# Performance work log

Hardware: AMD Instinct MI355X
Metric: run time of the kernel (lower is better)

## Reference

```python
import jax, jax.numpy as jnp
import numpy as np


def layer_norm(x, w, b, eps=1e-5):
    mu = jnp.mean(x, axis=-1, keepdims=True)
    var = jnp.mean(jnp.square(x - mu), axis=-1, keepdims=True)
    return (x - mu) / jnp.sqrt(var + eps) * w + b


def setup_inputs() -> dict:
    B, T, S, D, K = 8, 2048, 2048, 512, 3
    ks = jax.random.split(jax.random.key(0), 8)
    w_scale = 0.02  # modest init so softmax/layernorm stay in a sane range
    return {
        "x": jax.random.normal(ks[0], (B, T, D), jnp.float32),
        "enc": jax.random.normal(ks[1], (B, S, D), jnp.float32),
        "conv_w": jax.random.normal(ks[2], (2 * D, D, K), jnp.float32) * w_scale,
        "conv_b": jnp.zeros((2 * D,), jnp.float32),
        "ln1_w": jnp.ones((D,), jnp.float32),
        "ln1_b": jnp.zeros((D,), jnp.float32),
        "Wq": jax.random.normal(ks[3], (D, D), jnp.float32) * w_scale,
        "bq": jnp.zeros((D,), jnp.float32),
        "Wk": jax.random.normal(ks[4], (D, D), jnp.float32) * w_scale,
        "bk": jnp.zeros((D,), jnp.float32),
        "Wv": jax.random.normal(ks[5], (D, D), jnp.float32) * w_scale,
        "bv": jnp.zeros((D,), jnp.float32),
        "Wo": jax.random.normal(ks[6], (D, D), jnp.float32) * w_scale,
        "bo": jnp.zeros((D,), jnp.float32),
        "ln2_w": jnp.ones((D,), jnp.float32),
        "ln2_b": jnp.zeros((D,), jnp.float32),
    }


def reference(x, enc, conv_w, conv_b, ln1_w, ln1_b, Wq, bq, Wk, bk, Wv, bv, Wo, bo, ln2_w, ln2_b):
    D = x.shape[-1]
    K = conv_w.shape[-1]
    # Causal GLU: left-pad by K-1 so each output sees only past/current positions.
    xt = jnp.transpose(x, (0, 2, 1))  # [B, D, T]
    xt = jnp.pad(xt, ((0, 0), (0, 0), (K - 1, 0)))
    conv = jax.lax.conv_general_dilated(
        xt, conv_w, window_strides=(1,), padding="VALID",
        dimension_numbers=("NCH", "OIH", "NCH"))
    conv = conv + conv_b[None, :, None]
    conv = jnp.transpose(conv, (0, 2, 1))  # [B, T, 2D]
    a, g = jnp.split(conv, 2, axis=-1)
    glu = a * jax.nn.sigmoid(g)
    # residual + LN1 (dropout is identity in eval mode)
    h = layer_norm(glu + x, ln1_w, ln1_b)
    # cross-attention: bmm -> softmax -> bmm (single head)
    q = h @ Wq.T + bq            # [B, T, D]
    k = enc @ Wk.T + bk          # [B, S, D]
    v = enc @ Wv.T + bv          # [B, S, D]
    scores = jnp.einsum("btd,bsd->bts", q, k) / jnp.sqrt(jnp.float32(D))
    attn = jax.nn.softmax(scores, axis=-1)  # [B, T, S]
    ctx = jnp.einsum("bts,bsd->btd", attn, v)
    ctx = ctx @ Wo.T + bo
    out = layer_norm(h + ctx, ln2_w, ln2_b)
    return out, attn
```

## Files before the change

kernel.cpp:

```cpp
#include <hip/hip_runtime.h>
#include <hip/hip_bf16.h>
#include <stdint.h>


typedef unsigned short ushortT;
typedef __bf16 bf16x8 __attribute__((ext_vector_type(8)));
typedef float floatx4 __attribute__((ext_vector_type(4)));
typedef unsigned short ushort4v __attribute__((ext_vector_type(4)));
typedef unsigned short ushort8 __attribute__((ext_vector_type(8)));

__device__ __forceinline__ ushortT f2bf(float f) {
  unsigned u = __builtin_bit_cast(unsigned, f);
  u += 0x7FFFu + ((u >> 16) & 1u);
  return (ushortT)(u >> 16);
}
__device__ __forceinline__ float bf2f(ushortT u) {
  return __builtin_bit_cast(float, (unsigned)u << 16);
}

__device__ __forceinline__ void gload_lds16(const void* g, void* l) {
  __builtin_amdgcn_global_load_lds(
      (const __attribute__((address_space(1))) void*)g,
      (__attribute__((address_space(3))) void*)l, 16, 0, 0);
}

__global__ __launch_bounds__(256)
void k_f32_to_bf16v(const float* __restrict__ src, ushortT* __restrict__ dst, long n4) {
  long i = (long)blockIdx.x * 256 + threadIdx.x;
  if (i >= n4) return;
  floatx4 v = *(const floatx4*)&src[i * 4];
  ushort4v o;
#pragma unroll
  for (int j = 0; j < 4; j++) o[j] = f2bf(v[j]);
  *(ushort4v*)&dst[i * 4] = o;
}

__global__ __launch_bounds__(256)
void k_w4(const float* __restrict__ w0, const float* __restrict__ w1,
          const float* __restrict__ w2, const float* __restrict__ w3,
          ushortT* __restrict__ dst) {
  long i = (long)blockIdx.x * 256 + threadIdx.x;
  int m = (int)(i >> 16);
  long within = (i & 65535) * 4;
  const float* s = (m == 0) ? w0 : (m == 1) ? w1 : (m == 2) ? w2 : w3;
  floatx4 v = *(const floatx4*)&s[within];
  ushort4v o;
#pragma unroll
  for (int j = 0; j < 4; j++) o[j] = f2bf(v[j]);
  *(ushort4v*)&dst[(long)m * 262144 + within] = o;
}

__global__ __launch_bounds__(128)
void k_xpad(const float* __restrict__ x, ushortT* __restrict__ xp) {
  int row = blockIdx.x;
  int b = row / 2050, tp = row % 2050;
  int c = threadIdx.x * 4;
  ushort4v o = {0, 0, 0, 0};
  if (tp >= 2) {
    floatx4 v = *(const floatx4*)&x[((long)(b * 2048 + tp - 2)) * 512 + c];
#pragma unroll
    for (int j = 0; j < 4; j++) o[j] = f2bf(v[j]);
  }
  *(ushort4v*)&xp[(long)row * 512 + c] = o;
}

__global__ __launch_bounds__(256)
void k_convw(const float* __restrict__ w, ushortT* __restrict__ dst) {
  long idx = (long)blockIdx.x * 256 + threadIdx.x;
  if (idx >= 1024L * 1536) return;
  int n = (int)(idx / 1536), kk = (int)(idx % 1536);
  int tap = kk >> 9, i = kk & 511;
  int o = ((n >> 4) & 1) * 512 + (n >> 5) * 16 + (n & 15);
  dst[idx] = f2bf(w[(o * 512 + i) * 3 + tap]);
}

template<int CONV_A, int BIAS, int GLU, int WBF16, int SWAP = 0>
__global__ __launch_bounds__(256)
void k_gemm(const ushortT* __restrict__ A, long aBatch, int lda,
            const ushortT* __restrict__ Bm, long bBatch, int ldb,
            const float* __restrict__ bias, const float* __restrict__ xres,
            float* __restrict__ Cf, ushortT* __restrict__ Cb, long cBatch, int ldc,
            int Kdim, float scale)
{
  __shared__ ushortT As[128 * 32];
  __shared__ ushortT Bs[128 * 32];
  const int tid  = threadIdx.x;
  const int lane = tid & 63;
  const int wave = tid >> 6;
  const int wrow = (wave >> 1) * 64;
  const int wcol = (wave & 1) * 64;
  const int l15  = lane & 15;
  const int quad = lane >> 4;
  const long zA = (long)blockIdx.z * aBatch;
  const long zB = (long)blockIdx.z * bBatch;
  const long zC = (long)blockIdx.z * cBatch;
  const int rowBase = (SWAP ? blockIdx.y : blockIdx.x) * 128;
  const int colBase = (SWAP ? blockIdx.x : blockIdx.y) * 128;

  floatx4 zero = {0.f, 0.f, 0.f, 0.f};
  floatx4 acc[4][4];
#pragma unroll
  for (int mi = 0; mi < 4; mi++)
#pragma unroll
    for (int ni = 0; ni < 4; ni++) acc[mi][ni] = zero;

  for (int k0 = 0; k0 < Kdim; k0 += 32) {
    __syncthreads();
    {
      int ch = tid;
#pragma unroll
      for (int it = 0; it < 2; it++, ch += 256) {
        int row = ch >> 2, c8 = (ch & 3) << 3;
        if (CONV_A) {
          int gr = rowBase + row, gc = k0 + c8;
          int tap = gc >> 9, ii = gc & 511;
          int b = gr >> 11, t = gr & 2047;
          long gofs = ((long)(b * 2050 + t + tap) << 9) + ii;
          gload_lds16(A + gofs, &As[ch * 8]);
        } else {
          long gofs = zA + (long)(rowBase + row) * lda + (k0 + c8);
          gload_lds16(A + gofs, &As[ch * 8]);
        }
      }
      ch = tid;
#pragma unroll
      for (int it = 0; it < 2; it++, ch += 256) {
        int row = ch >> 2, c8 = (ch & 3) << 3;
        long gofs = zB + (long)(colBase + row) * ldb + (k0 + c8);
        gload_lds16(Bm + gofs, &Bs[ch * 8]);
      }
    }
    __syncthreads();
    bf16x8 av[4], bv[4];
#pragma unroll
    for (int mi = 0; mi < 4; mi++)
      av[mi] = *(const bf16x8*)&As[(wrow + mi * 16 + l15) * 32 + quad * 8];
#pragma unroll
    for (int ni = 0; ni < 4; ni++)
      bv[ni] = *(const bf16x8*)&Bs[(wcol + ni * 16 + l15) * 32 + quad * 8];
#pragma unroll
    for (int mi = 0; mi < 4; mi++)
#pragma unroll
      for (int ni = 0; ni < 4; ni++)
        acc[mi][ni] = __builtin_amdgcn_mfma_f32_16x16x32_bf16(av[mi], bv[ni], acc[mi][ni], 0, 0, 0);
  }

  if (GLU) {
#pragma unroll
    for (int mi = 0; mi < 4; mi++) {
#pragma unroll
      for (int ni = 0; ni < 4; ni += 2) {
        int colA = colBase + wcol + ni * 16;
        int d = (colA >> 5) * 16 + l15;
        float ba = bias[d], bg = bias[512 + d];
#pragma unroll
        for (int r = 0; r < 4; r++) {
          int grow = rowBase + wrow + mi * 16 + quad * 4 + r;
          float a = acc[mi][ni][r] + ba;
          float g = acc[mi][ni + 1][r] + bg;
          float val = a / (1.0f + __expf(-g)) + xres[(long)grow * 512 + d];
          Cf[(long)grow * 512 + d] = val;
        }
      }
    }
  } else {
#pragma unroll
    for (int mi = 0; mi < 4; mi++) {
#pragma unroll
      for (int ni = 0; ni < 4; ni++) {
        int gcol = colBase + wcol + ni * 16 + l15;
        float bcol = (BIAS == 1) ? bias[gcol] : 0.0f;
#pragma unroll
        for (int r = 0; r < 4; r++) {
          int grow = rowBase + wrow + mi * 16 + quad * 4 + r;
          float val = acc[mi][ni][r] * scale + bcol + ((BIAS == 2) ? bias[grow] : 0.0f);
          long off = zC + (long)grow * ldc + gcol;
          if (WBF16) Cb[off] = f2bf(val);
          else       Cf[off] = val;
        }
      }
    }
  }
}

template<int CONV_A, int GLU, int BIAS, int WBF16, int DUALZ, int SWAP>
__global__ __launch_bounds__(512)
void k_gemm256(const ushortT* __restrict__ A, const ushortT* __restrict__ A2, int lda, long aBatch,
               const ushortT* __restrict__ Bm, const ushortT* __restrict__ Bm2, int ldb, long bBatch,
               const float* __restrict__ bias, const float* __restrict__ bias2,
               const float* __restrict__ xres,
               float* __restrict__ Cf, ushortT* __restrict__ Cb, ushortT* __restrict__ Cb2,
               long cBatch, int ldc, int Kdim, float scale)
{
  __shared__ ushortT lds[2][2 * 16384];

  const int tid  = threadIdx.x;
  const int lane = tid & 63;
  const int wave = tid >> 6;
  const int wr   = wave >> 2;
  const int wc   = wave & 3;
  const int l15  = lane & 15;
  const int quad = lane >> 4;

  const ushortT* Ap = A;
  const ushortT* Bp = Bm;
  const float* biasP = bias;
  ushortT* CbP = Cb;
  if (DUALZ && blockIdx.z) { Ap = A2; Bp = Bm2; biasP = bias2; CbP = Cb2; }
  const long zA = DUALZ ? 0 : (long)blockIdx.z * aBatch;
  const long zB = DUALZ ? 0 : (long)blockIdx.z * bBatch;
  const long zC = DUALZ ? 0 : (long)blockIdx.z * cBatch;
  const int rowBase = (SWAP ? blockIdx.y : blockIdx.x) * 256;
  const int colBase = (SWAP ? blockIdx.x : blockIdx.y) * 256;

  auto STAGE = [&](int t) {
    ushortT* sA = lds[t & 1];
    ushortT* sB = sA + 16384;
    const int k0 = t << 6;
#pragma unroll
    for (int l = 0; l < 4; l++) {
      int idx = l * 512 + tid;
      int row = idx >> 3;
      int ck  = ((tid & 7) ^ (row & 7)) << 3;
      if (CONV_A) {
        int gr = rowBase + row;
        int gc = k0 + ck;
        int tap = gc >> 9, ii = gc & 511;
        int b = gr >> 11, tt = gr & 2047;
        long gofs = ((long)(b * 2050 + tt + tap) << 9) + ii;
        gload_lds16(Ap + gofs, sA + idx * 8);
      } else {
        long gofs = zA + (long)(rowBase + row) * lda + (k0 + ck);
        gload_lds16(Ap + gofs, sA + idx * 8);
      }
    }
#pragma unroll
    for (int l = 0; l < 4; l++) {
      int idx = l * 512 + tid;
      int row = idx >> 3;
      int ck  = ((tid & 7) ^ (row & 7)) << 3;
      long gofs = zB + (long)(colBase + row) * ldb + (k0 + ck);
      gload_lds16(Bp + gofs, sB + idx * 8);
    }
  };

  auto LD = [&](const ushortT* s, int r, int c) -> bf16x8 {
    return *(const bf16x8*)&s[r * 64 + ((c ^ (r & 7)) << 3)];
  };

  floatx4 zero = {0.f, 0.f, 0.f, 0.f};
  floatx4 acc[8][4];
#pragma unroll
  for (int mi = 0; mi < 8; mi++)
#pragma unroll
    for (int ni = 0; ni < 4; ni++) acc[mi][ni] = zero;

  const int NT = Kdim >> 6;
  STAGE(0);
  STAGE(1);

  for (int t = 0; t < NT; t++) {
    if (t < NT - 1) asm volatile("s_waitcnt vmcnt(8)" ::: "memory");
    else            asm volatile("s_waitcnt vmcnt(0)" ::: "memory");
    __builtin_amdgcn_s_barrier();

    const ushortT* sA = lds[t & 1];
    const ushortT* sB = sA + 16384;

    bf16x8 av[4][2], bv[4][2];
#pragma unroll
    for (int ni = 0; ni < 4; ni++)
#pragma unroll
      for (int ks = 0; ks < 2; ks++)
        bv[ni][ks] = LD(sB, wc * 64 + ni * 16 + l15, ks * 4 + quad);
#pragma unroll
    for (int mi = 0; mi < 4; mi++)
#pragma unroll
      for (int ks = 0; ks < 2; ks++)
        av[mi][ks] = LD(sA, wr * 128 + mi * 16 + l15, ks * 4 + quad);

    __builtin_amdgcn_s_setprio(1);
#pragma unroll
    for (int mi = 0; mi < 4; mi++)
#pragma unroll
      for (int ni = 0; ni < 4; ni++)
#pragma unroll
        for (int ks = 0; ks < 2; ks++)
          acc[mi][ni] = __builtin_amdgcn_mfma_f32_16x16x32_bf16(av[mi][ks], bv[ni][ks], acc[mi][ni], 0, 0, 0);
    __builtin_amdgcn_s_setprio(0);

#pragma unroll
    for (int mi = 0; mi < 4; mi++)
#pragma unroll
      for (int ks = 0; ks < 2; ks++)
        av[mi][ks] = LD(sA, wr * 128 + 64 + mi * 16 + l15, ks * 4 + quad);

    __builtin_amdgcn_s_setprio(1);
#pragma unroll
    for (int mi = 0; mi < 4; mi++)
#pragma unroll
      for (int ni = 0; ni < 4; ni++)
#pragma unroll
        for (int ks = 0; ks < 2; ks++)
          acc[4 + mi][ni] = __builtin_amdgcn_mfma_f32_16x16x32_bf16(av[mi][ks], bv[ni][ks], acc[4 + mi][ni], 0, 0, 0);
    __builtin_amdgcn_s_setprio(0);

    __builtin_amdgcn_s_barrier();
    if (t + 2 < NT) STAGE(t + 2);
  }

  if (GLU) {
#pragma unroll
    for (int mi = 0; mi < 8; mi++) {
#pragma unroll
      for (int ni = 0; ni < 4; ni += 2) {
        int colA = colBase + wc * 64 + ni * 16;
        int d = (colA >> 5) * 16 + l15;
        float ba = biasP[d], bg = biasP[512 + d];
#pragma unroll
        for (int r = 0; r < 4; r++) {
          int grow = rowBase + wr * 128 + mi * 16 + quad * 4 + r;
          float a = acc[mi][ni][r] + ba;
          float g = acc[mi][ni + 1][r] + bg;
          float val = a / (1.0f + __expf(-g)) + xres[(long)grow * 512 + d];
          Cf[(long)grow * 512 + d] = val;
        }
      }
    }
  } else {
#pragma unroll
    for (int mi = 0; mi < 8; mi++) {
#pragma unroll
      for (int ni = 0; ni < 4; ni++) {
        int gcol = colBase + wc * 64 + ni * 16 + l15;
        float bcol = BIAS ? biasP[gcol] : 0.0f;
#pragma unroll
        for (int r = 0; r < 4; r++) {
          int grow = rowBase + wr * 128 + mi * 16 + quad * 4 + r;
          float val = acc[mi][ni][r] * scale + bcol;
          long off = zC + (long)grow * ldc + gcol;
          if (WBF16) CbP[off] = f2bf(val);
          else       Cf[off] = val;
        }
      }
    }
  }
}

__global__ __launch_bounds__(128)
void k_ln(const float* __restrict__ src, const float* __restrict__ w, const float* __restrict__ b,
          ushortT* __restrict__ outb)
{
  __shared__ float s1[2], s2[2];
  long r = blockIdx.x;
  int tid = threadIdx.x;
  floatx4 v = *(const floatx4*)&src[r * 512 + tid * 4];
  float sum = v[0] + v[1] + v[2] + v[3];
  float ssq = v[0]*v[0] + v[1]*v[1] + v[2]*v[2] + v[3]*v[3];
#pragma unroll
  for (int off = 32; off; off >>= 1) { sum += __shfl_xor(sum, off); ssq += __shfl_xor(ssq, off); }
  if ((tid & 63) == 0) { s1[tid >> 6] = sum; s2[tid >> 6] = ssq; }
  __syncthreads();
  sum = s1[0] + s1[1]; ssq = s2[0] + s2[1];
  float mu = sum * (1.0f / 512.0f);
  float var = ssq * (1.0f / 512.0f) - mu * mu;
  float rstd = rsqrtf(var + 1e-5f);
  floatx4 wv = *(const floatx4*)&w[tid * 4];
  floatx4 bv = *(const floatx4*)&b[tid * 4];
  ushort4v ob;
#pragma unroll
  for (int j = 0; j < 4; j++) ob[j] = f2bf((v[j] - mu) * rstd * wv[j] + bv[j]);
  *(ushort4v*)&outb[r * 512 + tid * 4] = ob;
}

__global__ __launch_bounds__(256)
void k_softmax(ushortT* __restrict__ logits, float* __restrict__ attn)
{
  __shared__ float sred[4];
  long r = blockIdx.x;
  ushortT* lrow = logits + r * 2048;
  float* arow = attn + r * 2048;
  int tid = threadIdx.x;
  ushort8 uv = *(const ushort8*)&lrow[tid * 8];
  float v[8];
#pragma unroll
  for (int j = 0; j < 8; j++) v[j] = bf2f(uv[j]);
  float mx = v[0];
#pragma unroll
  for (int j = 1; j < 8; j++) mx = fmaxf(mx, v[j]);
#pragma unroll
  for (int off = 32; off; off >>= 1) mx = fmaxf(mx, __shfl_xor(mx, off));
  if ((tid & 63) == 0) sred[tid >> 6] = mx;
  __syncthreads();
  mx = fmaxf(fmaxf(sred[0], sred[1]), fmaxf(sred[2], sred[3]));
  __syncthreads();
  float sum = 0.f;
#pragma unroll
  for (int j = 0; j < 8; j++) { v[j] = __expf(v[j] - mx); sum += v[j]; }
#pragma unroll
  for (int off = 32; off; off >>= 1) sum += __shfl_xor(sum, off);
  if ((tid & 63) == 0) sred[tid >> 6] = sum;
  __syncthreads();
  sum = sred[0] + sred[1] + sred[2] + sred[3];
  float inv = 1.0f / sum;
  floatx4 o0, o1;
  ushort8 ob;
#pragma unroll
  for (int j = 0; j < 8; j++) {
    float p = v[j] * inv;
    if (j < 4) o0[j] = p; else o1[j - 4] = p;
    ob[j] = f2bf(p);
  }
  *(floatx4*)&arow[tid * 8] = o0;
  *(floatx4*)&arow[tid * 8 + 4] = o1;
  *(ushort8*)&lrow[tid * 8] = ob;
}

__global__ __launch_bounds__(256)
void k_oproj_ln(const ushortT* __restrict__ ctx, const ushortT* __restrict__ Wo,
                const float* __restrict__ bo, const ushortT* __restrict__ h,
                const float* __restrict__ w, const float* __restrict__ b,
                float* __restrict__ out)
{
  __shared__ ushortT As[32 * 32];
  __shared__ ushortT Bs[512 * 32];
  __shared__ float psum[4][32], pssq[4][32];
  const int tid = threadIdx.x, lane = tid & 63, wave = tid >> 6;
  const int l15 = lane & 15, quad = lane >> 4;
  const int rowBase = blockIdx.x * 32;

  floatx4 zero = {0.f, 0.f, 0.f, 0.f};
  floatx4 acc[2][8];
#pragma unroll
  for (int mi = 0; mi < 2; mi++)
#pragma unroll
    for (int ni = 0; ni < 8; ni++) acc[mi][ni] = zero;

  for (int k0 = 0; k0 < 512; k0 += 32) {
    __syncthreads();
    if (tid < 128)
      gload_lds16(ctx + (long)(rowBase + (tid >> 2)) * 512 + k0 + ((tid & 3) << 3), &As[tid * 8]);
#pragma unroll
    for (int it = 0; it < 8; it++) {
      int ch = tid + it * 256;
      gload_lds16(Wo + (long)(ch >> 2) * 512 + k0 + ((ch & 3) << 3), &Bs[ch * 8]);
    }
    __syncthreads();
    bf16x8 av[2], bv[8];
#pragma unroll
    for (int mi = 0; mi < 2; mi++)
      av[mi] = *(const bf16x8*)&As[(mi * 16 + l15) * 32 + quad * 8];
#pragma unroll
    for (int ni = 0; ni < 8; ni++)
      bv[ni] = *(const bf16x8*)&Bs[(wave * 128 + ni * 16 + l15) * 32 + quad * 8];
#pragma unroll
    for (int mi = 0; mi < 2; mi++)
#pragma unroll
      for (int ni = 0; ni < 8; ni++)
        acc[mi][ni] = __builtin_amdgcn_mfma_f32_16x16x32_bf16(av[mi], bv[ni], acc[mi][ni], 0, 0, 0);
  }

  float lnw[8], lnb[8], bov[8];
#pragma unroll
  for (int ni = 0; ni < 8; ni++) {
    int col = wave * 128 + ni * 16 + l15;
    bov[ni] = bo[col]; lnw[ni] = w[col]; lnb[ni] = b[col];
  }
#pragma unroll
  for (int mi = 0; mi < 2; mi++) {
#pragma unroll
    for (int r = 0; r < 4; r++) {
      long grow = rowBase + mi * 16 + quad * 4 + r;
      float ps = 0.f, pq = 0.f;
#pragma unroll
      for (int ni = 0; ni < 8; ni++) {
        int col = wave * 128 + ni * 16 + l15;
        float val = acc[mi][ni][r] + bov[ni] + bf2f(h[grow * 512 + col]);
        acc[mi][ni][r] = val;
        ps += val; pq += val * val;
      }
#pragma unroll
      for (int off = 1; off < 16; off <<= 1) { ps += __shfl_xor(ps, off); pq += __shfl_xor(pq, off); }
      if (l15 == 0) { int rl = mi * 16 + quad * 4 + r; psum[wave][rl] = ps; pssq[wave][rl] = pq; }
    }
  }
  __syncthreads();
#pragma unroll
  for (int mi = 0; mi < 2; mi++) {
#pragma unroll
    for (int r = 0; r < 4; r++) {
      int rl = mi * 16 + quad * 4 + r;
      float S = psum[0][rl] + psum[1][rl] + psum[2][rl] + psum[3][rl];
      float Q = pssq[0][rl] + pssq[1][rl] + pssq[2][rl] + pssq[3][rl];
      float mu = S * (1.0f / 512.0f);
      float rstd = rsqrtf(Q * (1.0f / 512.0f) - mu * mu + 1e-5f);
      long grow = rowBase + rl;
#pragma unroll
      for (int ni = 0; ni < 8; ni++) {
        int col = wave * 128 + ni * 16 + l15;
        out[grow * 512 + col] = (acc[mi][ni][r] - mu) * rstd * lnw[ni] + lnb[ni];
      }
    }
  }
}

extern "C" void kernel_launch(void* const* d_in, const int* in_sizes, int n_in,
                              void* d_out, int out_size, void* d_ws, size_t ws_size,
                              hipStream_t stream)
{
  const float* x      = (const float*)d_in[0];
  const float* enc    = (const float*)d_in[1];
  const float* conv_w = (const float*)d_in[2];
  const float* conv_b = (const float*)d_in[3];
  const float* ln1_w  = (const float*)d_in[4];
  const float* ln1_b  = (const float*)d_in[5];
  const float* Wq     = (const float*)d_in[6];
  const float* bq     = (const float*)d_in[7];
  const float* Wk     = (const float*)d_in[8];
  const float* bk     = (const float*)d_in[9];
  const float* Wv     = (const float*)d_in[10];
  const float* bv     = (const float*)d_in[11];
  const float* Wo     = (const float*)d_in[12];
  const float* bo     = (const float*)d_in[13];
  const float* ln2_w  = (const float*)d_in[14];
  const float* ln2_b  = (const float*)d_in[15];

  const long BT = 16384, Dd = 512, S = 2048, TT = 2048;
  float* out  = (float*)d_out;
  float* attn = out + BT * Dd;

  char* p = (char*)d_ws;
  auto alloc = [&](size_t bytes) { char* r = p; p += (bytes + 255) & ~255UL; return r; };
  float*   hglu  = (float*)alloc(BT * Dd * 4);
  ushortT* xpad  = (ushortT*)alloc(8L * 2050 * 512 * 2);
  ushortT* encbf = (ushortT*)alloc(BT * Dd * 2);
  ushortT* hbf   = (ushortT*)alloc(BT * Dd * 2);
  ushortT* qbf   = (ushortT*)alloc(BT * Dd * 2);
  ushortT* kbf   = (ushortT*)alloc(BT * Dd * 2);
  ushortT* vT    = (ushortT*)alloc(Dd * BT * 2);
  ushortT* ctxbf = (ushortT*)alloc(BT * Dd * 2);
  ushortT* sl    = (ushortT*)alloc(BT * S * 2);
  ushortT* Wcbf  = (ushortT*)alloc(1024L * 1536 * 2);
  ushortT* wall  = (ushortT*)alloc(4L * 262144 * 2);
  ushortT* Wqbf = wall, *Wkbf = wall + 262144, *Wvbf = wall + 2 * 262144, *Wobf = wall + 3 * 262144;

  k_xpad<<<8 * 2050, 128, 0, stream>>>(x, xpad);
  k_f32_to_bf16v<<<(BT * Dd / 4 + 255) / 256, 256, 0, stream>>>(enc, encbf, BT * Dd / 4);
  k_convw<<<(1024 * 1536 + 255) / 256, 256, 0, stream>>>(conv_w, Wcbf);
  k_w4<<<1024, 256, 0, stream>>>(Wq, Wk, Wv, Wo, wall);

  k_gemm256<1, 1, 0, 0, 0, 0><<<dim3(64, 4, 1), 512, 0, stream>>>(
      xpad, nullptr, 0, 0, Wcbf, nullptr, 1536, 0,
      conv_b, nullptr, x, hglu, nullptr, nullptr, 0, 512, 1536, 1.0f);
  k_ln<<<16384, 128, 0, stream>>>(hglu, ln1_w, ln1_b, hbf);

  k_gemm256<0, 0, 1, 1, 1, 0><<<dim3(64, 2, 2), 512, 0, stream>>>(
      hbf, encbf, 512, 0, Wqbf, Wkbf, 512, 0,
      bq, bk, nullptr, nullptr, qbf, kbf, 0, 512, 512, 1.0f);

  k_gemm<0, 2, 0, 1><<<dim3(4, 128), 256, 0, stream>>>(
      Wvbf, 0, 512, encbf, 0, 512, bv, nullptr, nullptr, vT, 0, 16384, 512, 1.0f);

  k_gemm256<0, 0, 0, 1, 0, 0><<<dim3(8, 8, 8), 512, 0, stream>>>(
      qbf, nullptr, 512, TT * Dd, kbf, nullptr, 512, S * Dd,
      nullptr, nullptr, nullptr, nullptr, sl, nullptr,
      TT * S, 2048, 512, 0.04419417382415922f);
  k_softmax<<<16384, 256, 0, stream>>>(sl, attn);

  k_gemm256<0, 0, 0, 1, 0, 1><<<dim3(2, 8, 8), 512, 0, stream>>>(
      sl, nullptr, 2048, TT * S, vT, nullptr, 16384, TT,
      nullptr, nullptr, nullptr, nullptr, ctxbf, nullptr,
      TT * Dd, 512, 2048, 1.0f);

  k_oproj_ln<<<512, 256, 0, stream>>>(ctxbf, Wobf, bo, hbf, ln2_w, ln2_b, out);
}
```

Before: 526.9 us.

## Add double-buffered 64x512 GEMM kernel for V-proj, PV and O-proj+LN

Introduces a new GEMM kernel with 64-row by 512-column tiles, a K-step of 64, an XOR-swizzled LDS layout and two-stage global_load_lds prefetch with vmcnt waits and setprio around the MFMAs. It replaces the old 128x128 V-projection kernel, the 256-tile attention-times-V GEMM and the separate O-projection+LN2 kernel, which becomes an epilogue mode of the new kernel. The aim is to overlap loads with compute, cut LDS bank conflicts and use a shape suited to N=512 outputs. The risks are the large LDS footprint (about 144 KB per block) limiting occupancy, and the PV GEMM now launching only 256 blocks.

```diff
diff --git a/kernel.cpp b/kernel.cpp
--- a/kernel.cpp
+++ b/kernel.cpp
@@ -72,115 +72,6 @@
   int tap = kk >> 9, i = kk & 511;
   int o = ((n >> 4) & 1) * 512 + (n >> 5) * 16 + (n & 15);
   dst[idx] = f2bf(w[(o * 512 + i) * 3 + tap]);
-}
-
-template<int CONV_A, int BIAS, int GLU, int WBF16, int SWAP = 0>
-__global__ __launch_bounds__(256)
-void k_gemm(const ushortT* __restrict__ A, long aBatch, int lda,
-            const ushortT* __restrict__ Bm, long bBatch, int ldb,
-            const float* __restrict__ bias, const float* __restrict__ xres,
-            float* __restrict__ Cf, ushortT* __restrict__ Cb, long cBatch, int ldc,
-            int Kdim, float scale)
-{
-  __shared__ ushortT As[128 * 32];
-  __shared__ ushortT Bs[128 * 32];
-  const int tid  = threadIdx.x;
-  const int lane = tid & 63;
-  const int wave = tid >> 6;
-  const int wrow = (wave >> 1) * 64;
-  const int wcol = (wave & 1) * 64;
-  const int l15  = lane & 15;
-  const int quad = lane >> 4;
-  const long zA = (long)blockIdx.z * aBatch;
-  const long zB = (long)blockIdx.z * bBatch;
-  const long zC = (long)blockIdx.z * cBatch;
-  const int rowBase = (SWAP ? blockIdx.y : blockIdx.x) * 128;
-  const int colBase = (SWAP ? blockIdx.x : blockIdx.y) * 128;
-
-  floatx4 zero = {0.f, 0.f, 0.f, 0.f};
-  floatx4 acc[4][4];
-#pragma unroll
-  for (int mi = 0; mi < 4; mi++)
-#pragma unroll
-    for (int ni = 0; ni < 4; ni++) acc[mi][ni] = zero;
-
-  for (int k0 = 0; k0 < Kdim; k0 += 32) {
-    __syncthreads();
-    {
-      int ch = tid;
-#pragma unroll
-      for (int it = 0; it < 2; it++, ch += 256) {
-        int row = ch >> 2, c8 = (ch & 3) << 3;
-        if (CONV_A) {
-          int gr = rowBase + row, gc = k0 + c8;
-          int tap = gc >> 9, ii = gc & 511;
-          int b = gr >> 11, t = gr & 2047;
-          long gofs = ((long)(b * 2050 + t + tap) << 9) + ii;
-          gload_lds16(A + gofs, &As[ch * 8]);
-        } else {
-          long gofs = zA + (long)(rowBase + row) * lda + (k0 + c8);
-          gload_lds16(A + gofs, &As[ch * 8]);
-        }
-      }
-      ch = tid;
-#pragma unroll
-      for (int it = 0; it < 2; it++, ch += 256) {
-        int row = ch >> 2, c8 = (ch & 3) << 3;
-        long gofs = zB + (long)(colBase + row) * ldb + (k0 + c8);
-        gload_lds16(Bm + gofs, &Bs[ch * 8]);
-      }
-    }
-    __syncthreads();
-    bf16x8 av[4], bv[4];
-#pragma unroll
-    for (int mi = 0; mi < 4; mi++)
-      av[mi] = *(const bf16x8*)&As[(wrow + mi * 16 + l15) * 32 + quad * 8];
-#pragma unroll
-    for (int ni = 0; ni < 4; ni++)
-      bv[ni] = *(const bf16x8*)&Bs[(wcol + ni * 16 + l15) * 32 + quad * 8];
-#pragma unroll
-    for (int mi = 0; mi < 4; mi++)
-#pragma unroll
-      for (int ni = 0; ni < 4; ni++)
-        acc[mi][ni] = __builtin_amdgcn_mfma_f32_16x16x32_bf16(av[mi], bv[ni], acc[mi][ni], 0, 0, 0);
-  }
-
-  if (GLU) {
-#pragma unroll
-    for (int mi = 0; mi < 4; mi++) {
-#pragma unroll
-      for (int ni = 0; ni < 4; ni += 2) {
-        int colA = colBase + wcol + ni * 16;
-        int d = (colA >> 5) * 16 + l15;
-        float ba = bias[d], bg = bias[512 + d];
-#pragma unroll
-        for (int r = 0; r < 4; r++) {
-          int grow = rowBase + wrow + mi * 16 + quad * 4 + r;
-          float a = acc[mi][ni][r] + ba;
-          float g = acc[mi][ni + 1][r] + bg;
-          float val = a / (1.0f + __expf(-g)) + xres[(long)grow * 512 + d];
-          Cf[(long)grow * 512 + d] = val;
-        }
-      }
-    }
-  } else {
-#pragma unroll
-    for (int mi = 0; mi < 4; mi++) {
-#pragma unroll
-      for (int ni = 0; ni < 4; ni++) {
-        int gcol = colBase + wcol + ni * 16 + l15;
-        float bcol = (BIAS == 1) ? bias[gcol] : 0.0f;
-#pragma unroll
-        for (int r = 0; r < 4; r++) {
-          int grow = rowBase + wrow + mi * 16 + quad * 4 + r;
-          float val = acc[mi][ni][r] * scale + bcol + ((BIAS == 2) ? bias[grow] : 0.0f);
-          long off = zC + (long)grow * ldc + gcol;
-          if (WBF16) Cb[off] = f2bf(val);
-          else       Cf[off] = val;
-        }
-      }
-    }
-  }
 }
 
 template<int CONV_A, int GLU, int BIAS, int WBF16, int DUALZ, int SWAP>
@@ -347,6 +238,166 @@
   }
 }
 
+template<int BIAS, int WBF16, int LNEPI>
+__global__ __launch_bounds__(512)
+void k_gemm64(const ushortT* __restrict__ A, int lda, long aBatch,
+              const ushortT* __restrict__ Bm, int ldb, long bBatch,
+              const float* __restrict__ bias, const ushortT* __restrict__ hres,
+              const float* __restrict__ lnw, const float* __restrict__ lnb,
+              float* __restrict__ Cf, ushortT* __restrict__ Cb,
+              long cBatch, int ldc, int Kdim, float scale)
+{
+  __shared__ ushortT lds[2][(64 + 512) * 64];
+
+  const int tid  = threadIdx.x;
+  const int lane = tid & 63;
+  const int wave = tid >> 6;
+  const int l15  = lane & 15;
+  const int quad = lane >> 4;
+
+  const long zA = (long)blockIdx.z * aBatch;
+  const long zB = (long)blockIdx.z * bBatch;
+  const long zC = (long)blockIdx.z * cBatch;
+  const int rowBase = blockIdx.y * 64;
+  const int colBase = blockIdx.x * 512;
+
+  auto STAGE = [&](int t) {
+    ushortT* sA = lds[t & 1];
+    ushortT* sB = sA + 64 * 64;
+    const int k0 = t << 6;
+    {
+      int row = tid >> 3;
+      int ck  = ((tid & 7) ^ (row & 7)) << 3;
+      long gofs = zA + (long)(rowBase + row) * lda + (k0 + ck);
+      gload_lds16(A + gofs, sA + tid * 8);
+    }
+#pragma unroll
+    for (int l = 0; l < 8; l++) {
+      int idx = l * 512 + tid;
+      int row = idx >> 3;
+      int ck  = ((tid & 7) ^ (row & 7)) << 3;
+      long gofs = zB + (long)(colBase + row) * ldb + (k0 + ck);
+      gload_lds16(Bm + gofs, sB + idx * 8);
+    }
+  };
+
+  auto LD = [&](const ushortT* s, int r, int c) -> bf16x8 {
+    return *(const bf16x8*)&s[r * 64 + ((c ^ (r & 7)) << 3)];
+  };
+
+  floatx4 zero = {0.f, 0.f, 0.f, 0.f};
+  floatx4 acc[4][4];
+#pragma unroll
+  for (int mi = 0; mi < 4; mi++)
+#pragma unroll
+    for (int ni = 0; ni < 4; ni++) acc[mi][ni] = zero;
+
+  const int NT = Kdim >> 6;
+  STAGE(0);
+  STAGE(1);
+
+  for (int t = 0; t < NT; t++) {
+    if (t < NT - 1) asm volatile("s_waitcnt vmcnt(9)" ::: "memory");
+    else            asm volatile("s_waitcnt vmcnt(0)" ::: "memory");
+    __builtin_amdgcn_s_barrier();
+
+    const ushortT* sA = lds[t & 1];
+    const ushortT* sB = sA + 64 * 64;
+
+    bf16x8 av[4][2], bv[4][2];
+#pragma unroll
+    for (int ni = 0; ni < 4; ni++)
+#pragma unroll
+      for (int ks = 0; ks < 2; ks++)
+        bv[ni][ks] = LD(sB, wave * 64 + ni * 16 + l15, ks * 4 + quad);
+#pragma unroll
+    for (int mi = 0; mi < 4; mi++)
+#pragma unroll
+      for (int ks = 0; ks < 2; ks++)
+        av[mi][ks] = LD(sA, mi * 16 + l15, ks * 4 + quad);
+
+    __builtin_amdgcn_s_setprio(1);
+#pragma unroll
+    for (int mi = 0; mi < 4; mi++)
+#pragma unroll
+      for (int ni = 0; ni < 4; ni++)
+#pragma unroll
+        for (int ks = 0; ks < 2; ks++)
+          acc[mi][ni] = __builtin_amdgcn_mfma_f32_16x16x32_bf16(av[mi][ks], bv[ni][ks], acc[mi][ni], 0, 0, 0);
+    __builtin_amdgcn_s_setprio(0);
+
+    __builtin_amdgcn_s_barrier();
+    if (t + 2 < NT) STAGE(t + 2);
+  }
+
+  if (LNEPI) {
+    float bov[4], lw[4], lb[4];
+#pragma unroll
+    for (int ni = 0; ni < 4; ni++) {
+      int col = wave * 64 + ni * 16 + l15;
+      bov[ni] = bias[col]; lw[ni] = lnw[col]; lb[ni] = lnb[col];
+    }
+    float* psum = (float*)&lds[0][0];
+    float* pssq = psum + 8 * 64;
+    __syncthreads();
+#pragma unroll
+    for (int mi = 0; mi < 4; mi++) {
+#pragma unroll
+      for (int r = 0; r < 4; r++) {
+        int rowl = mi * 16 + quad * 4 + r;
+        long grow = rowBase + rowl;
+        float ps = 0.f, pq = 0.f;
+#pragma unroll
+        for (int ni = 0; ni < 4; ni++) {
+          int col = wave * 64 + ni * 16 + l15;
+          float val = acc[mi][ni][r] + bov[ni] + bf2f(hres[grow * 512 + col]);
+          acc[mi][ni][r] = val;
+          ps += val; pq += val * val;
+        }
+#pragma unroll
+        for (int off = 1; off < 16; off <<= 1) { ps += __shfl_xor(ps, off); pq += __shfl_xor(pq, off); }
+        if (l15 == 0) { psum[wave * 64 + rowl] = ps; pssq[wave * 64 + rowl] = pq; }
+      }
+    }
+    __syncthreads();
+#pragma unroll
+    for (int mi = 0; mi < 4; mi++) {
+#pragma unroll
+      for (int r = 0; r < 4; r++) {
+        int rowl = mi * 16 + quad * 4 + r;
+        float S = 0.f, Q = 0.f;
+#pragma unroll
+        for (int w = 0; w < 8; w++) { S += psum[w * 64 + rowl]; Q += pssq[w * 64 + rowl]; }
+        float mu = S * (1.0f / 512.0f);
+        float rstd = rsqrtf(Q * (1.0f / 512.0f) - mu * mu + 1e-5f);
+        long grow = rowBase + rowl;
+#pragma unroll
+        for (int ni = 0; ni < 4; ni++) {
+          int col = wave * 64 + ni * 16 + l15;
+          Cf[grow * 512 + col] = (acc[mi][ni][r] - mu) * rstd * lw[ni] + lb[ni];
+        }
+      }
+    }
+  } else {
+#pragma unroll
+    for (int mi = 0; mi < 4; mi++) {
+#pragma unroll
+      for (int ni = 0; ni < 4; ni++) {
+        int gcol = colBase + wave * 64 + ni * 16 + l15;
+        float bcol = (BIAS == 1) ? bias[gcol] : 0.0f;
+#pragma unroll
+        for (int r = 0; r < 4; r++) {
+          int grow = rowBase + mi * 16 + quad * 4 + r;
+          float val = acc[mi][ni][r] * scale + bcol + ((BIAS == 2) ? bias[grow] : 0.0f);
+          long off = zC + (long)grow * ldc + gcol;
+          if (WBF16) Cb[off] = f2bf(val);
+          else       Cf[off] = val;
+        }
+      }
+    }
+  }
+}
+
 __global__ __launch_bounds__(128)
 void k_ln(const float* __restrict__ src, const float* __restrict__ w, const float* __restrict__ b,
           ushortT* __restrict__ outb)
@@ -414,94 +465,6 @@
   *(floatx4*)&arow[tid * 8] = o0;
   *(floatx4*)&arow[tid * 8 + 4] = o1;
   *(ushort8*)&lrow[tid * 8] = ob;
-}
-
-__global__ __launch_bounds__(256)
-void k_oproj_ln(const ushortT* __restrict__ ctx, const ushortT* __restrict__ Wo,
-                const float* __restrict__ bo, const ushortT* __restrict__ h,
-                const float* __restrict__ w, const float* __restrict__ b,
-                float* __restrict__ out)
-{
-  __shared__ ushortT As[32 * 32];
-  __shared__ ushortT Bs[512 * 32];
-  __shared__ float psum[4][32], pssq[4][32];
-  const int tid = threadIdx.x, lane = tid & 63, wave = tid >> 6;
-  const int l15 = lane & 15, quad = lane >> 4;
-  const int rowBase = blockIdx.x * 32;
-
-  floatx4 zero = {0.f, 0.f, 0.f, 0.f};
-  floatx4 acc[2][8];
-#pragma unroll
-  for (int mi = 0; mi < 2; mi++)
-#pragma unroll
-    for (int ni = 0; ni < 8; ni++) acc[mi][ni] = zero;
-
-  for (int k0 = 0; k0 < 512; k0 += 32) {
-    __syncthreads();
-    if (tid < 128)
-      gload_lds16(ctx + (long)(rowBase + (tid >> 2)) * 512 + k0 + ((tid & 3) << 3), &As[tid * 8]);
-#pragma unroll
-    for (int it = 0; it < 8; it++) {
-      int ch = tid + it * 256;
-      gload_lds16(Wo + (long)(ch >> 2) * 512 + k0 + ((ch & 3) << 3), &Bs[ch * 8]);
-    }
-    __syncthreads();
-    bf16x8 av[2], bv[8];
-#pragma unroll
-    for (int mi = 0; mi < 2; mi++)
-      av[mi] = *(const bf16x8*)&As[(mi * 16 + l15) * 32 + quad * 8];
-#pragma unroll
-    for (int ni = 0; ni < 8; ni++)
-      bv[ni] = *(const bf16x8*)&Bs[(wave * 128 + ni * 16 + l15) * 32 + quad * 8];
-#pragma unroll
-    for (int mi = 0; mi < 2; mi++)
-#pragma unroll
-      for (int ni = 0; ni < 8; ni++)
-        acc[mi][ni] = __builtin_amdgcn_mfma_f32_16x16x32_bf16(av[mi], bv[ni], acc[mi][ni], 0, 0, 0);
-  }
-
-  float lnw[8], lnb[8], bov[8];
-#pragma unroll
-  for (int ni = 0; ni < 8; ni++) {
-    int col = wave * 128 + ni * 16 + l15;
-    bov[ni] = bo[col]; lnw[ni] = w[col]; lnb[ni] = b[col];
-  }
-#pragma unroll
-  for (int mi = 0; mi < 2; mi++) {
-#pragma unroll
-    for (int r = 0; r < 4; r++) {
-      long grow = rowBase + mi * 16 + quad * 4 + r;
-      float ps = 0.f, pq = 0.f;
-#pragma unroll
-      for (int ni = 0; ni < 8; ni++) {
-        int col = wave * 128 + ni * 16 + l15;
-        float val = acc[mi][ni][r] + bov[ni] + bf2f(h[grow * 512 + col]);
-        acc[mi][ni][r] = val;
-        ps += val; pq += val * val;
-      }
-#pragma unroll
-      for (int off = 1; off < 16; off <<= 1) { ps += __shfl_xor(ps, off); pq += __shfl_xor(pq, off); }
-      if (l15 == 0) { int rl = mi * 16 + quad * 4 + r; psum[wave][rl] = ps; pssq[wave][rl] = pq; }
-    }
-  }
-  __syncthreads();
-#pragma unroll
-  for (int mi = 0; mi < 2; mi++) {
-#pragma unroll
-    for (int r = 0; r < 4; r++) {
-      int rl = mi * 16 + quad * 4 + r;
-      float S = psum[0][rl] + psum[1][rl] + psum[2][rl] + psum[3][rl];
-      float Q = pssq[0][rl] + pssq[1][rl] + pssq[2][rl] + pssq[3][rl];
-      float mu = S * (1.0f / 512.0f);
-      float rstd = rsqrtf(Q * (1.0f / 512.0f) - mu * mu + 1e-5f);
-      long grow = rowBase + rl;
-#pragma unroll
-      for (int ni = 0; ni < 8; ni++) {
-        int col = wave * 128 + ni * 16 + l15;
-        out[grow * 512 + col] = (acc[mi][ni][r] - mu) * rstd * lnw[ni] + lnb[ni];
-      }
-    }
-  }
 }
 
 extern "C" void kernel_launch(void* const* d_in, const int* in_sizes, int n_in,
@@ -558,8 +521,10 @@
       hbf, encbf, 512, 0, Wqbf, Wkbf, 512, 0,
       bq, bk, nullptr, nullptr, qbf, kbf, 0, 512, 512, 1.0f);
 
-  k_gemm<0, 2, 0, 1><<<dim3(4, 128), 256, 0, stream>>>(
-      Wvbf, 0, 512, encbf, 0, 512, bv, nullptr, nullptr, vT, 0, 16384, 512, 1.0f);
+  k_gemm64<2, 1, 0><<<dim3(32, 8, 1), 512, 0, stream>>>(
+      Wvbf, 512, 0, encbf, 512, 0,
+      bv, nullptr, nullptr, nullptr,
+      nullptr, vT, 0, 16384, 512, 1.0f);
 
   k_gemm256<0, 0, 0, 1, 0, 0><<<dim3(8, 8, 8), 512, 0, stream>>>(
       qbf, nullptr, 512, TT * Dd, kbf, nullptr, 512, S * Dd,
@@ -567,10 +532,13 @@
       TT * S, 2048, 512, 0.04419417382415922f);
   k_softmax<<<16384, 256, 0, stream>>>(sl, attn);
 
-  k_gemm256<0, 0, 0, 1, 0, 1><<<dim3(2, 8, 8), 512, 0, stream>>>(
-      sl, nullptr, 2048, TT * S, vT, nullptr, 16384, TT,
-      nullptr, nullptr, nullptr, nullptr, ctxbf, nullptr,
-      TT * Dd, 512, 2048, 1.0f);
-
-  k_oproj_ln<<<512, 256, 0, stream>>>(ctxbf, Wobf, bo, hbf, ln2_w, ln2_b, out);
-}
+  k_gemm64<0, 1, 0><<<dim3(1, 32, 8), 512, 0, stream>>>(
+      sl, 2048, TT * S, vT, 16384, TT,
+      nullptr, nullptr, nullptr, nullptr,
+      nullptr, ctxbf, TT * Dd, 512, 2048, 1.0f);
+
+  k_gemm64<0, 0, 1><<<dim3(1, 256, 1), 512, 0, stream>>>(
+      ctxbf, 512, 0, Wobf, 512, 0,
+      bo, hbf, ln2_w, ln2_b,
+      out, nullptr, 0, 512, 512, 1.0f);
+}
```

Result: no change. 531.2 us (+0.8%).
